# Kernel tuning notes

Measured on AMD Instinct MI355X. Metric: run time of the kernel, lower is better.

Reference implementation:

```python
import jax, jax.numpy as jnp
import numpy as np

B, C, N = 4, 256, 2048
H = 8
HD = C // H  # head_dim = 32


def setup_inputs() -> dict:
    key = jax.random.key(0)
    ks = jax.random.split(key, 5)
    s = 1.0 / np.sqrt(C)
    return {
        "x": jax.random.normal(ks[0], (B, C, 3, N), dtype=jnp.float32),
        "Wq": jax.random.normal(ks[1], (C, C), dtype=jnp.float32) * s,
        "Wk": jax.random.normal(ks[2], (C, C), dtype=jnp.float32) * s,
        "Wv": jax.random.normal(ks[3], (C, C), dtype=jnp.float32) * s,
        "Wo": jax.random.normal(ks[4], (C, C), dtype=jnp.float32) * s,
    }


def _vn_linear(W, x):
    # nn.Linear over channel axis: out[b,o,d,n] = sum_c W[o,c] x[b,c,d,n]
    return jnp.einsum('oc,bcdn->bodn', W, x)


def _heads(t):
    # [B,C,3,N] -> [B,H,N,HD,3]
    return t.reshape(B, H, HD, 3, N).transpose(0, 1, 4, 2, 3)


def reference(x, Wq, Wk, Wv, Wo):
    q = _heads(_vn_linear(Wq, x))
    k = _heads(_vn_linear(Wk, x))
    v = _heads(_vn_linear(Wv, x))
    # energy contracts over (head_dim, 3)
    energy = jnp.einsum('bhnci,bhmci->bhnm', q, k)
    attn = jax.nn.softmax(energy / np.sqrt(HD), axis=-1)
    out = jnp.einsum('bhnm,bhmci->bhnci', attn, v)
    # [B,H,N,HD,3] -> [B,C,3,N]
    out = out.transpose(0, 1, 3, 4, 2).reshape(B, C, 3, N)
    out = _vn_linear(Wo, out)
    return out + x
```

## Files before the change

kernel.cpp:

```cpp
#include <hip/hip_runtime.h>
#include <hip/hip_bf16.h>
#include <cmath>


typedef unsigned short u16;
typedef unsigned int   u32;
typedef u16   u16x8  __attribute__((ext_vector_type(8)));
typedef short s16x8  __attribute__((ext_vector_type(8)));
typedef float f32x4  __attribute__((ext_vector_type(4)));
typedef float f32x16 __attribute__((ext_vector_type(16)));

namespace {
constexpr int Nc = 2048, Fc = 96;
constexpr float SCALE_LOG2 = 0.17677669529663687f * 1.4426950408889634f;
constexpr float DEFER_THR  = 8.0f;
constexpr int KP = 104;
constexpr int VP = 40;
constexpr int VOFF = 32 * KP;
constexpr int SBUF = VOFF + 96 * VP;
}

__device__ inline float fast_exp2(float x) {
#if __has_builtin(__builtin_amdgcn_exp2f)
    return __builtin_amdgcn_exp2f(x);
#else
    return exp2f(x);
#endif
}

__device__ inline u16 f2bf(float x) {
    union { float f; unsigned u; } v; v.f = x;
    unsigned r = v.u + 0x7FFFu + ((v.u >> 16) & 1u);
    return (u16)(r >> 16);
}

__global__ __launch_bounds__(256) void wconv_kernel(
    const float* __restrict__ Wq, const float* __restrict__ Wk,
    const float* __restrict__ Wv, const float* __restrict__ Wo,
    u16* __restrict__ Wb)
{
    const int id = blockIdx.x * 256 + threadIdx.x;
    const int base = id * 8;
    const int o = base >> 8, c = base & 255;
    const int sel = o >> 8, ol = o & 255;
    const float* src = (sel == 0) ? Wq : (sel == 1) ? Wk : (sel == 2) ? Wv : Wo;
    const float sc = (sel == 0) ? SCALE_LOG2 : 1.0f;
    const float4 a = *(const float4*)&src[(size_t)ol * 256 + c];
    const float4 b = *(const float4*)&src[(size_t)ol * 256 + c + 4];
    u16x8 r;
    r[0]=f2bf(a.x*sc); r[1]=f2bf(a.y*sc); r[2]=f2bf(a.z*sc); r[3]=f2bf(a.w*sc);
    r[4]=f2bf(b.x*sc); r[5]=f2bf(b.y*sc); r[6]=f2bf(b.z*sc); r[7]=f2bf(b.w*sc);
    *(u16x8*)&Wb[(size_t)o * 256 + c] = r;
}

__global__ __launch_bounds__(256) void xt_kernel(
    const float* __restrict__ x, u16* __restrict__ xt)
{
    const int nt = blockIdx.x, ct = blockIdx.y, bi = blockIdx.z;
    const int b = bi / 3, i = bi % 3;
    const int t = (int)threadIdx.x;
    const int n0 = nt * 64, c0 = ct * 64;

    __shared__ u16 tile[64][72];

    const int n_l = t & 63;
#pragma unroll
    for (int it = 0; it < 16; ++it) {
        const int c_l = (t >> 6) + it * 4;
        tile[n_l][c_l] =
            f2bf(x[(((size_t)(b * 256 + c0 + c_l)) * 3 + i) * Nc + n0 + n_l]);
    }
    __syncthreads();
#pragma unroll
    for (int it = 0; it < 2; ++it) {
        const int idx = t + it * 256;
        const int nn = idx >> 3, part = idx & 7;
        *(u16x8*)&xt[((size_t)bi * Nc + n0 + nn) * 256 + c0 + part * 8] =
            *(const u16x8*)&tile[nn][part * 8];
    }
}

__global__ __launch_bounds__(256) void qkv_gemm_kernel(
    const u16* __restrict__ xt, const u16* __restrict__ wb,
    u16* __restrict__ Qt, u16* __restrict__ Kt, u16* __restrict__ Vf)
{
    const int nt = blockIdx.x;
    const int wy = blockIdx.y;
    const int bi = blockIdx.z;
    const int b = bi / 3, i = bi % 3;
    const int wsel = wy >> 1, ot = wy & 1;

    const u16* xs = xt + ((size_t)bi * Nc + nt * 128) * 256;
    const u16* ws = wb + (size_t)(wsel * 256 + ot * 128) * 256;

    __shared__ u16 xl[128][40];
    __shared__ u16 wl[128][40];

    const int t = (int)threadIdx.x;
    const int wv = t >> 6, lane = t & 63;
    const int g = lane >> 4, c16 = lane & 15;
    const int wr = wv >> 1, wc = wv & 1;

    f32x4 acc[4][4];
#pragma unroll
    for (int mi = 0; mi < 4; ++mi)
#pragma unroll
        for (int ni = 0; ni < 4; ++ni)
#pragma unroll
            for (int r = 0; r < 4; ++r) acc[mi][ni][r] = 0.f;

    for (int ks = 0; ks < 8; ++ks) {
        __syncthreads();
#pragma unroll
        for (int it = 0; it < 2; ++it) {
            const int idx = t + it * 256;
            const int row = idx >> 2, part = idx & 3;
            *(u16x8*)&xl[row][part * 8] =
                *(const u16x8*)&xs[(size_t)row * 256 + ks * 32 + part * 8];
            *(u16x8*)&wl[row][part * 8] =
                *(const u16x8*)&ws[(size_t)row * 256 + ks * 32 + part * 8];
        }
        __syncthreads();

        s16x8 af[4], bf[4];
        if (wsel < 2) {
#pragma unroll
            for (int mi = 0; mi < 4; ++mi) af[mi] = *(const s16x8*)&xl[wr*64 + mi*16 + c16][g*8];
#pragma unroll
            for (int ni = 0; ni < 4; ++ni) bf[ni] = *(const s16x8*)&wl[wc*64 + ni*16 + c16][g*8];
        } else {
#pragma unroll
            for (int mi = 0; mi < 4; ++mi) af[mi] = *(const s16x8*)&wl[wr*64 + mi*16 + c16][g*8];
#pragma unroll
            for (int ni = 0; ni < 4; ++ni) bf[ni] = *(const s16x8*)&xl[wc*64 + ni*16 + c16][g*8];
        }
#pragma unroll
        for (int mi = 0; mi < 4; ++mi)
#pragma unroll
            for (int ni = 0; ni < 4; ++ni)
                acc[mi][ni] = __builtin_amdgcn_mfma_f32_16x16x32_bf16(
                    af[mi], bf[ni], acc[mi][ni], 0, 0, 0);
    }

    if (wsel < 2) {
        u16* dst = wsel ? Kt : Qt;
#pragma unroll
        for (int mi = 0; mi < 4; ++mi)
#pragma unroll
            for (int ni = 0; ni < 4; ++ni) {
                const int o = ot * 128 + wc * 64 + ni * 16 + c16;
                const int h = o >> 5, cw = o & 31;
#pragma unroll
                for (int r = 0; r < 4; ++r) {
                    const int n = nt * 128 + wr * 64 + mi * 16 + g * 4 + r;
                    dst[((size_t)(b * 8 + h) * Nc + n) * Fc + i * 32 + cw] =
                        f2bf(acc[mi][ni][r]);
                }
            }
    } else {
#pragma unroll
        for (int mi = 0; mi < 4; ++mi)
#pragma unroll
            for (int ni = 0; ni < 4; ++ni) {
                const int n = nt * 128 + wc * 64 + ni * 16 + c16;
#pragma unroll
                for (int r = 0; r < 4; ++r) {
                    const int o = ot * 128 + wr * 64 + mi * 16 + g * 4 + r;
                    const int h = o >> 5, cw = o & 31;
                    Vf[((size_t)(b * 8 + h) * Fc + i * 32 + cw) * Nc + n] =
                        f2bf(acc[mi][ni][r]);
                }
            }
    }
}

__global__ __launch_bounds__(256) void attn_mfma_kernel(
    const u16* __restrict__ Qt, const u16* __restrict__ Kt,
    const u16* __restrict__ Vf, u16* __restrict__ AO)
{
    const int bid = (int)blockIdx.x;
    const int lid = (bid & 7) * 64 + (bid >> 3);
    const int bh = lid >> 4;
    const int qt = lid & 15;

    const int t    = (int)threadIdx.x;
    const int wq   = t >> 6;
    const int lane = t & 63;
    const int ql   = lane & 31;
    const int hi   = lane >> 5;

    __shared__ u16 sbuf[2][SBUF];

    const int qb = qt * 128 + wq * 32;

    s16x8 bq[6];
#pragma unroll
    for (int s6 = 0; s6 < 6; ++s6)
        bq[s6] = *(const s16x8*)&Qt[((size_t)bh * Nc + qb + ql) * Fc + s6 * 16 + hi * 8];

    const u16* g_src[3]; int g_str[3], g_dst[3];
#pragma unroll
    for (int it = 0; it < 3; ++it) {
        const int c = t + it * 256;
        if (c < 384) {
            const int row = c / 12, part = c - row * 12;
            g_src[it] = Kt + ((size_t)bh * Nc + row) * Fc + part * 8;
            g_str[it] = 32 * Fc;
            g_dst[it] = row * KP + part * 8;
        } else {
            const int c2 = c - 384, f = c2 >> 2, part = c2 & 3;
            g_src[it] = Vf + ((size_t)bh * Fc + f) * Nc + part * 8;
            g_str[it] = 32;
            g_dst[it] = VOFF + f * VP + part * 8;
        }
    }

    f32x16 acc[3];
#pragma unroll
    for (int ft = 0; ft < 3; ++ft)
#pragma unroll
        for (int r = 0; r < 16; ++r) acc[ft][r] = 0.f;
    float m_s = -INFINITY, l_s = 0.f;

    u16x8 streg[3];
#pragma unroll
    for (int it = 0; it < 3; ++it) streg[it] = *(const u16x8*)g_src[it];
#pragma unroll
    for (int it = 0; it < 3; ++it) *(u16x8*)&sbuf[0][g_dst[it]] = streg[it];
    __syncthreads();

    for (int kt = 0; kt < 64; ++kt) {
        const int cur = kt & 1;
        if (kt < 63) {
#pragma unroll
            for (int it = 0; it < 3; ++it)
                streg[it] = *(const u16x8*)(g_src[it] + (size_t)(kt + 1) * g_str[it]);
        }

        const u16* kb = &sbuf[cur][0];
        const u16* vb = &sbuf[cur][VOFF];

        f32x16 sv;
#pragma unroll
        for (int r = 0; r < 16; ++r) sv[r] = 0.f;
#pragma unroll
        for (int s6 = 0; s6 < 6; ++s6) {
            const s16x8 ka = *(const s16x8*)&kb[ql * KP + s6 * 16 + hi * 8];
            sv = __builtin_amdgcn_mfma_f32_32x32x16_bf16(ka, bq[s6], sv, 0, 0, 0);
        }

        float mloc = sv[0];
#pragma unroll
        for (int r = 1; r < 16; ++r) mloc = fmaxf(mloc, sv[r]);
        mloc = fmaxf(mloc, __shfl_xor(mloc, 32));

        if (__any(mloc > m_s + DEFER_THR)) {
            const float mnew = fmaxf(m_s, mloc);
            const float esc = fast_exp2(m_s - mnew);
            m_s = mnew; l_s *= esc;
#pragma unroll
            for (int ft = 0; ft < 3; ++ft)
#pragma unroll
                for (int r = 0; r < 16; ++r) acc[ft][r] *= esc;
        }

        float p[16]; float lsum = 0.f;
#pragma unroll
        for (int r = 0; r < 16; ++r) { p[r] = fast_exp2(sv[r] - m_s); lsum += p[r]; }
        lsum += __shfl_xor(lsum, 32);
        l_s += lsum;

        u32 pk8[8];
#pragma unroll
        for (int j = 0; j < 8; ++j)
            asm("v_cvt_pk_bf16_f32 %0, %1, %2" : "=v"(pk8[j]) : "v"(p[2*j]), "v"(p[2*j+1]));
        asm volatile("v_permlane32_swap_b32 %0, %1" : "+v"(pk8[0]), "+v"(pk8[2]));
        asm volatile("v_permlane32_swap_b32 %0, %1" : "+v"(pk8[1]), "+v"(pk8[3]));
        asm volatile("v_permlane32_swap_b32 %0, %1" : "+v"(pk8[4]), "+v"(pk8[6]));
        asm volatile("v_permlane32_swap_b32 %0, %1" : "+v"(pk8[5]), "+v"(pk8[7]));
        union U { u32 w[4]; s16x8 v; } pb0, pb1;
        pb0.w[0] = pk8[0]; pb0.w[1] = pk8[1]; pb0.w[2] = pk8[2]; pb0.w[3] = pk8[3];
        pb1.w[0] = pk8[4]; pb1.w[1] = pk8[5]; pb1.w[2] = pk8[6]; pb1.w[3] = pk8[7];

#pragma unroll
        for (int ft = 0; ft < 3; ++ft) {
            const s16x8 va0 = *(const s16x8*)&vb[(ft * 32 + ql) * VP + hi * 8];
            acc[ft] = __builtin_amdgcn_mfma_f32_32x32x16_bf16(va0, pb0.v, acc[ft], 0, 0, 0);
            const s16x8 va1 = *(const s16x8*)&vb[(ft * 32 + ql) * VP + 16 + hi * 8];
            acc[ft] = __builtin_amdgcn_mfma_f32_32x32x16_bf16(va1, pb1.v, acc[ft], 0, 0, 0);
        }

        if (kt < 63) {
#pragma unroll
            for (int it = 0; it < 3; ++it) *(u16x8*)&sbuf[cur ^ 1][g_dst[it]] = streg[it];
        }
        __syncthreads();
    }

    const float inv = 1.f / l_s;
#pragma unroll
    for (int ft = 0; ft < 3; ++ft)
#pragma unroll
        for (int r = 0; r < 16; ++r) {
            const int frow = (r & 3) + 8 * (r >> 2) + 4 * hi;
            AO[((size_t)bh * Fc + ft * 32 + frow) * Nc + qb + ql] =
                f2bf(acc[ft][r] * inv);
        }
}

__global__ __launch_bounds__(256) void aot_kernel(
    const u16* __restrict__ aof, u16* __restrict__ aot)
{
    const int nt = blockIdx.x, i = blockIdx.y, bh = blockIdx.z;
    const int b = bh >> 3, h = bh & 7;
    const int t = (int)threadIdx.x;
    const int n0 = nt * 64;

    __shared__ u16 tile[64][40];

    const int n_l = t & 63;
#pragma unroll
    for (int it = 0; it < 8; ++it) {
        const int f_l = (t >> 6) + it * 4;
        tile[n_l][f_l] = aof[((size_t)bh * Fc + i * 32 + f_l) * Nc + n0 + n_l];
    }
    __syncthreads();
    const int nn = t >> 2, part = t & 3;
    *(u16x8*)&aot[((size_t)(b * 3 + i) * Nc + n0 + nn) * 256 + h * 32 + part * 8] =
        *(const u16x8*)&tile[nn][part * 8];
}

__global__ __launch_bounds__(256) void out_gemm_kernel(
    const u16* __restrict__ aot, const u16* __restrict__ wb,
    const float* __restrict__ x, float* __restrict__ out)
{
    const int nt = blockIdx.x, ot = blockIdx.y, bi = blockIdx.z;
    const int b = bi / 3, i = bi % 3;

    const u16* bs = aot + ((size_t)bi * Nc + nt * 128) * 256;
    const u16* ws = wb + (size_t)(768 + ot * 128) * 256;

    __shared__ u16 al[128][40];
    __shared__ u16 wl[128][40];

    const int t = (int)threadIdx.x;
    const int wv = t >> 6, lane = t & 63;
    const int g = lane >> 4, c16 = lane & 15;
    const int wr = wv >> 1, wc = wv & 1;

    f32x4 acc[4][4];
#pragma unroll
    for (int mi = 0; mi < 4; ++mi)
#pragma unroll
        for (int ni = 0; ni < 4; ++ni)
#pragma unroll
            for (int r = 0; r < 4; ++r) acc[mi][ni][r] = 0.f;

    for (int ks = 0; ks < 8; ++ks) {
        __syncthreads();
#pragma unroll
        for (int it = 0; it < 2; ++it) {
            const int idx = t + it * 256;
            const int row = idx >> 2, part = idx & 3;
            *(u16x8*)&al[row][part * 8] =
                *(const u16x8*)&bs[(size_t)row * 256 + ks * 32 + part * 8];
            *(u16x8*)&wl[row][part * 8] =
                *(const u16x8*)&ws[(size_t)row * 256 + ks * 32 + part * 8];
        }
        __syncthreads();

        s16x8 af[4], bf[4];
#pragma unroll
        for (int mi = 0; mi < 4; ++mi) af[mi] = *(const s16x8*)&wl[wr*64 + mi*16 + c16][g*8];
#pragma unroll
        for (int ni = 0; ni < 4; ++ni) bf[ni] = *(const s16x8*)&al[wc*64 + ni*16 + c16][g*8];
#pragma unroll
        for (int mi = 0; mi < 4; ++mi)
#pragma unroll
            for (int ni = 0; ni < 4; ++ni)
                acc[mi][ni] = __builtin_amdgcn_mfma_f32_16x16x32_bf16(
                    af[mi], bf[ni], acc[mi][ni], 0, 0, 0);
    }

#pragma unroll
    for (int mi = 0; mi < 4; ++mi)
#pragma unroll
        for (int ni = 0; ni < 4; ++ni) {
            const int n = nt * 128 + wc * 64 + ni * 16 + c16;
#pragma unroll
            for (int r = 0; r < 4; ++r) {
                const int o = ot * 128 + wr * 64 + mi * 16 + g * 4 + r;
                const size_t idx = ((size_t)(b * 256 + o) * 3 + i) * Nc + n;
                out[idx] = x[idx] + acc[mi][ni][r];
            }
        }
}

extern "C" void kernel_launch(void* const* d_in, const int* in_sizes, int n_in,
                              void* d_out, int out_size, void* d_ws, size_t ws_size,
                              hipStream_t stream) {
    const float* x  = (const float*)d_in[0];
    const float* Wq = (const float*)d_in[1];
    const float* Wk = (const float*)d_in[2];
    const float* Wv = (const float*)d_in[3];
    const float* Wo = (const float*)d_in[4];
    float* out = (float*)d_out;

    const size_t E = (size_t)32 * Fc * Nc;
    u16* xt  = (u16*)d_ws;
    u16* wbw = xt + E;
    u16* qt  = wbw + 262144;
    u16* kt  = qt + E;
    u16* vf  = kt + E;
    u16* aof = vf + E;
    u16* aot = aof + E;

    dim3 blk(256);
    wconv_kernel    <<<dim3(128),        blk, 0, stream>>>(Wq, Wk, Wv, Wo, wbw);
    xt_kernel       <<<dim3(32, 4, 12),  blk, 0, stream>>>(x, xt);
    qkv_gemm_kernel <<<dim3(16, 6, 12),  blk, 0, stream>>>(xt, wbw, qt, kt, vf);
    attn_mfma_kernel<<<dim3(512),        blk, 0, stream>>>(qt, kt, vf, aof);
    aot_kernel      <<<dim3(32, 3, 32),  blk, 0, stream>>>(aof, aot);
    out_gemm_kernel <<<dim3(16, 2, 12),  blk, 0, stream>>>(aot, wbw, x, out);
}
```

Measured before the change: 138.2 us.

## Double KV tile size in attention, fuse output transpose, and add prefetch depth

The attention kernel now processes 64 keys per iteration with two score MFMA chains, halving the loop count and the number of barriers. Global loads are issued two tiles ahead, with stores to the alternate LDS buffer done at the top of each iteration. Tree reductions replace the serial max and sum, and s_setprio raises wave priority around the MFMA sections. The separate aot transpose kernel is removed: attention output is staged through LDS and written directly in the layout the output GEMM expects, which drops one launch and one global round trip at the cost of more LDS and registers per block.

```diff
diff --git a/kernel.cpp b/kernel.cpp
--- a/kernel.cpp
+++ b/kernel.cpp
@@ -15,8 +15,8 @@
 constexpr float SCALE_LOG2 = 0.17677669529663687f * 1.4426950408889634f;
 constexpr float DEFER_THR  = 8.0f;
 constexpr int KP = 104;
-constexpr int VP = 40;
-constexpr int VOFF = 32 * KP;
+constexpr int VP = 72;
+constexpr int VOFF = 64 * KP;
 constexpr int SBUF = VOFF + 96 * VP;
 }
 
@@ -176,7 +176,7 @@
 
 __global__ __launch_bounds__(256) void attn_mfma_kernel(
     const u16* __restrict__ Qt, const u16* __restrict__ Kt,
-    const u16* __restrict__ Vf, u16* __restrict__ AO)
+    const u16* __restrict__ Vf, u16* __restrict__ aot)
 {
     const int bid = (int)blockIdx.x;
     const int lid = (bid & 7) * 64 + (bid >> 3);
@@ -198,19 +198,20 @@
     for (int s6 = 0; s6 < 6; ++s6)
         bq[s6] = *(const s16x8*)&Qt[((size_t)bh * Nc + qb + ql) * Fc + s6 * 16 + hi * 8];
 
-    const u16* g_src[3]; int g_str[3], g_dst[3];
-#pragma unroll
-    for (int it = 0; it < 3; ++it) {
-        const int c = t + it * 256;
-        if (c < 384) {
+    const u16* g_src[6]; int g_str[6], g_dst[6];
+#pragma unroll
+    for (int it = 0; it < 6; ++it) {
+        if (it < 3) {
+            const int c = t + it * 256;
             const int row = c / 12, part = c - row * 12;
             g_src[it] = Kt + ((size_t)bh * Nc + row) * Fc + part * 8;
-            g_str[it] = 32 * Fc;
+            g_str[it] = 64 * Fc;
             g_dst[it] = row * KP + part * 8;
         } else {
-            const int c2 = c - 384, f = c2 >> 2, part = c2 & 3;
+            const int c = t + (it - 3) * 256;
+            const int f = c >> 3, part = c & 7;
             g_src[it] = Vf + ((size_t)bh * Fc + f) * Nc + part * 8;
-            g_str[it] = 32;
+            g_str[it] = 64;
             g_dst[it] = VOFF + f * VP + part * 8;
         }
     }
@@ -222,37 +223,52 @@
         for (int r = 0; r < 16; ++r) acc[ft][r] = 0.f;
     float m_s = -INFINITY, l_s = 0.f;
 
-    u16x8 streg[3];
-#pragma unroll
-    for (int it = 0; it < 3; ++it) streg[it] = *(const u16x8*)g_src[it];
-#pragma unroll
-    for (int it = 0; it < 3; ++it) *(u16x8*)&sbuf[0][g_dst[it]] = streg[it];
+    u16x8 sreg[6];
+#pragma unroll
+    for (int it = 0; it < 6; ++it) sreg[it] = *(const u16x8*)g_src[it];
+#pragma unroll
+    for (int it = 0; it < 6; ++it) *(u16x8*)&sbuf[0][g_dst[it]] = sreg[it];
+#pragma unroll
+    for (int it = 0; it < 6; ++it)
+        sreg[it] = *(const u16x8*)(g_src[it] + (size_t)g_str[it]);
     __syncthreads();
 
-    for (int kt = 0; kt < 64; ++kt) {
+    for (int kt = 0; kt < 32; ++kt) {
         const int cur = kt & 1;
-        if (kt < 63) {
-#pragma unroll
-            for (int it = 0; it < 3; ++it)
-                streg[it] = *(const u16x8*)(g_src[it] + (size_t)(kt + 1) * g_str[it]);
+        if (kt < 31) {
+#pragma unroll
+            for (int it = 0; it < 6; ++it) *(u16x8*)&sbuf[cur ^ 1][g_dst[it]] = sreg[it];
+        }
+        if (kt < 30) {
+#pragma unroll
+            for (int it = 0; it < 6; ++it)
+                sreg[it] = *(const u16x8*)(g_src[it] + (size_t)(kt + 2) * g_str[it]);
         }
 
         const u16* kb = &sbuf[cur][0];
         const u16* vb = &sbuf[cur][VOFF];
 
-        f32x16 sv;
-#pragma unroll
-        for (int r = 0; r < 16; ++r) sv[r] = 0.f;
+        f32x16 sv0, sv1;
+#pragma unroll
+        for (int r = 0; r < 16; ++r) { sv0[r] = 0.f; sv1[r] = 0.f; }
+        __builtin_amdgcn_s_setprio(1);
 #pragma unroll
         for (int s6 = 0; s6 < 6; ++s6) {
-            const s16x8 ka = *(const s16x8*)&kb[ql * KP + s6 * 16 + hi * 8];
-            sv = __builtin_amdgcn_mfma_f32_32x32x16_bf16(ka, bq[s6], sv, 0, 0, 0);
-        }
-
-        float mloc = sv[0];
-#pragma unroll
-        for (int r = 1; r < 16; ++r) mloc = fmaxf(mloc, sv[r]);
-        mloc = fmaxf(mloc, __shfl_xor(mloc, 32));
+            const s16x8 ka0 = *(const s16x8*)&kb[ql * KP + s6 * 16 + hi * 8];
+            sv0 = __builtin_amdgcn_mfma_f32_32x32x16_bf16(ka0, bq[s6], sv0, 0, 0, 0);
+            const s16x8 ka1 = *(const s16x8*)&kb[(32 + ql) * KP + s6 * 16 + hi * 8];
+            sv1 = __builtin_amdgcn_mfma_f32_32x32x16_bf16(ka1, bq[s6], sv1, 0, 0, 0);
+        }
+        __builtin_amdgcn_s_setprio(0);
+
+        float mx[16];
+#pragma unroll
+        for (int r = 0; r < 16; ++r) mx[r] = fmaxf(sv0[r], sv1[r]);
+#pragma unroll
+        for (int s = 8; s > 0; s >>= 1)
+#pragma unroll
+            for (int r = 0; r < 16; ++r) if (r < s) mx[r] = fmaxf(mx[r], mx[r + s]);
+        const float mloc = fmaxf(mx[0], __shfl_xor(mx[0], 32));
 
         if (__any(mloc > m_s + DEFER_THR)) {
             const float mnew = fmaxf(m_s, mloc);
@@ -264,70 +280,90 @@
                 for (int r = 0; r < 16; ++r) acc[ft][r] *= esc;
         }
 
-        float p[16]; float lsum = 0.f;
-#pragma unroll
-        for (int r = 0; r < 16; ++r) { p[r] = fast_exp2(sv[r] - m_s); lsum += p[r]; }
-        lsum += __shfl_xor(lsum, 32);
-        l_s += lsum;
-
-        u32 pk8[8];
-#pragma unroll
-        for (int j = 0; j < 8; ++j)
-            asm("v_cvt_pk_bf16_f32 %0, %1, %2" : "=v"(pk8[j]) : "v"(p[2*j]), "v"(p[2*j+1]));
-        asm volatile("v_permlane32_swap_b32 %0, %1" : "+v"(pk8[0]), "+v"(pk8[2]));
-        asm volatile("v_permlane32_swap_b32 %0, %1" : "+v"(pk8[1]), "+v"(pk8[3]));
-        asm volatile("v_permlane32_swap_b32 %0, %1" : "+v"(pk8[4]), "+v"(pk8[6]));
-        asm volatile("v_permlane32_swap_b32 %0, %1" : "+v"(pk8[5]), "+v"(pk8[7]));
-        union U { u32 w[4]; s16x8 v; } pb0, pb1;
-        pb0.w[0] = pk8[0]; pb0.w[1] = pk8[1]; pb0.w[2] = pk8[2]; pb0.w[3] = pk8[3];
-        pb1.w[0] = pk8[4]; pb1.w[1] = pk8[5]; pb1.w[2] = pk8[6]; pb1.w[3] = pk8[7];
-
+#pragma unroll
+        for (int r = 0; r < 16; ++r) {
+            sv0[r] = fast_exp2(sv0[r] - m_s);
+            sv1[r] = fast_exp2(sv1[r] - m_s);
+        }
+        float ls[16];
+#pragma unroll
+        for (int r = 0; r < 16; ++r) ls[r] = sv0[r] + sv1[r];
+#pragma unroll
+        for (int s = 8; s > 0; s >>= 1)
+#pragma unroll
+            for (int r = 0; r < 16; ++r) if (r < s) ls[r] += ls[r + s];
+        l_s += ls[0] + __shfl_xor(ls[0], 32);
+
+        u32 pk0[8], pk1[8];
+#pragma unroll
+        for (int j = 0; j < 8; ++j) {
+            asm("v_cvt_pk_bf16_f32 %0, %1, %2" : "=v"(pk0[j]) : "v"(sv0[2*j]), "v"(sv0[2*j+1]));
+            asm("v_cvt_pk_bf16_f32 %0, %1, %2" : "=v"(pk1[j]) : "v"(sv1[2*j]), "v"(sv1[2*j+1]));
+        }
+        asm volatile("v_permlane32_swap_b32 %0, %1" : "+v"(pk0[0]), "+v"(pk0[2]));
+        asm volatile("v_permlane32_swap_b32 %0, %1" : "+v"(pk0[1]), "+v"(pk0[3]));
+        asm volatile("v_permlane32_swap_b32 %0, %1" : "+v"(pk0[4]), "+v"(pk0[6]));
+        asm volatile("v_permlane32_swap_b32 %0, %1" : "+v"(pk0[5]), "+v"(pk0[7]));
+        asm volatile("v_permlane32_swap_b32 %0, %1" : "+v"(pk1[0]), "+v"(pk1[2]));
+        asm volatile("v_permlane32_swap_b32 %0, %1" : "+v"(pk1[1]), "+v"(pk1[3]));
+        asm volatile("v_permlane32_swap_b32 %0, %1" : "+v"(pk1[4]), "+v"(pk1[6]));
+        asm volatile("v_permlane32_swap_b32 %0, %1" : "+v"(pk1[5]), "+v"(pk1[7]));
+        union U { u32 w[4]; s16x8 v; } pb[4];
+        pb[0].w[0]=pk0[0]; pb[0].w[1]=pk0[1]; pb[0].w[2]=pk0[2]; pb[0].w[3]=pk0[3];
+        pb[1].w[0]=pk0[4]; pb[1].w[1]=pk0[5]; pb[1].w[2]=pk0[6]; pb[1].w[3]=pk0[7];
+        pb[2].w[0]=pk1[0]; pb[2].w[1]=pk1[1]; pb[2].w[2]=pk1[2]; pb[2].w[3]=pk1[3];
+        pb[3].w[0]=pk1[4]; pb[3].w[1]=pk1[5]; pb[3].w[2]=pk1[6]; pb[3].w[3]=pk1[7];
+
+        __builtin_amdgcn_s_setprio(1);
 #pragma unroll
         for (int ft = 0; ft < 3; ++ft) {
-            const s16x8 va0 = *(const s16x8*)&vb[(ft * 32 + ql) * VP + hi * 8];
-            acc[ft] = __builtin_amdgcn_mfma_f32_32x32x16_bf16(va0, pb0.v, acc[ft], 0, 0, 0);
-            const s16x8 va1 = *(const s16x8*)&vb[(ft * 32 + ql) * VP + 16 + hi * 8];
-            acc[ft] = __builtin_amdgcn_mfma_f32_32x32x16_bf16(va1, pb1.v, acc[ft], 0, 0, 0);
-        }
-
-        if (kt < 63) {
-#pragma unroll
-            for (int it = 0; it < 3; ++it) *(u16x8*)&sbuf[cur ^ 1][g_dst[it]] = streg[it];
-        }
+#pragma unroll
+            for (int ks = 0; ks < 4; ++ks) {
+                const s16x8 va = *(const s16x8*)&vb[(ft * 32 + ql) * VP + ks * 16 + hi * 8];
+                acc[ft] = __builtin_amdgcn_mfma_f32_32x32x16_bf16(va, pb[ks].v, acc[ft], 0, 0, 0);
+            }
+        }
+        __builtin_amdgcn_s_setprio(0);
+
         __syncthreads();
     }
 
     const float inv = 1.f / l_s;
+    u16* ot = &sbuf[0][0] + wq * (32 * 104);
 #pragma unroll
     for (int ft = 0; ft < 3; ++ft)
 #pragma unroll
         for (int r = 0; r < 16; ++r) {
             const int frow = (r & 3) + 8 * (r >> 2) + 4 * hi;
-            AO[((size_t)bh * Fc + ft * 32 + frow) * Nc + qb + ql] =
-                f2bf(acc[ft][r] * inv);
-        }
-}
-
-__global__ __launch_bounds__(256) void aot_kernel(
-    const u16* __restrict__ aof, u16* __restrict__ aot)
-{
-    const int nt = blockIdx.x, i = blockIdx.y, bh = blockIdx.z;
-    const int b = bh >> 3, h = bh & 7;
-    const int t = (int)threadIdx.x;
-    const int n0 = nt * 64;
-
-    __shared__ u16 tile[64][40];
-
-    const int n_l = t & 63;
-#pragma unroll
-    for (int it = 0; it < 8; ++it) {
-        const int f_l = (t >> 6) + it * 4;
-        tile[n_l][f_l] = aof[((size_t)bh * Fc + i * 32 + f_l) * Nc + n0 + n_l];
-    }
+            ot[ql * 104 + ft * 32 + frow] = f2bf(acc[ft][r] * inv);
+        }
     __syncthreads();
-    const int nn = t >> 2, part = t & 3;
-    *(u16x8*)&aot[((size_t)(b * 3 + i) * Nc + n0 + nn) * 256 + h * 32 + part * 8] =
-        *(const u16x8*)&tile[nn][part * 8];
+
+    u16x8 v6[6];
+#pragma unroll
+    for (int j = 0; j < 6; ++j)
+        v6[j] = *(const u16x8*)&ot[ql * 104 + hi * 48 + j * 8];
+
+    const int n = qb + ql;
+    const int b_ = bh >> 3, h_ = bh & 7;
+    const size_t base0 = ((size_t)(b_ * 3 + 0) * Nc + n) * 256 + h_ * 32;
+    const size_t base1 = ((size_t)(b_ * 3 + 1) * Nc + n) * 256 + h_ * 32;
+    const size_t base2 = ((size_t)(b_ * 3 + 2) * Nc + n) * 256 + h_ * 32;
+    if (hi == 0) {
+        *(u16x8*)&aot[base0 +  0] = v6[0];
+        *(u16x8*)&aot[base0 +  8] = v6[1];
+        *(u16x8*)&aot[base0 + 16] = v6[2];
+        *(u16x8*)&aot[base0 + 24] = v6[3];
+        *(u16x8*)&aot[base1 +  0] = v6[4];
+        *(u16x8*)&aot[base1 +  8] = v6[5];
+    } else {
+        *(u16x8*)&aot[base1 + 16] = v6[0];
+        *(u16x8*)&aot[base1 + 24] = v6[1];
+        *(u16x8*)&aot[base2 +  0] = v6[2];
+        *(u16x8*)&aot[base2 +  8] = v6[3];
+        *(u16x8*)&aot[base2 + 16] = v6[4];
+        *(u16x8*)&aot[base2 + 24] = v6[5];
+    }
 }
 
 __global__ __launch_bounds__(256) void out_gemm_kernel(
@@ -412,14 +448,12 @@
     u16* qt  = wbw + 262144;
     u16* kt  = qt + E;
     u16* vf  = kt + E;
-    u16* aof = vf + E;
-    u16* aot = aof + E;
+    u16* aot = vf + E;
 
     dim3 blk(256);
     wconv_kernel    <<<dim3(128),        blk, 0, stream>>>(Wq, Wk, Wv, Wo, wbw);
     xt_kernel       <<<dim3(32, 4, 12),  blk, 0, stream>>>(x, xt);
     qkv_gemm_kernel <<<dim3(16, 6, 12),  blk, 0, stream>>>(xt, wbw, qt, kt, vf);
-    attn_mfma_kernel<<<dim3(512),        blk, 0, stream>>>(qt, kt, vf, aof);
-    aot_kernel      <<<dim3(32, 3, 32),  blk, 0, stream>>>(aof, aot);
+    attn_mfma_kernel<<<dim3(512),        blk, 0, stream>>>(qt, kt, vf, aot);
     out_gemm_kernel <<<dim3(16, 2, 12),  blk, 0, stream>>>(aot, wbw, x, out);
 }
```

Result: no change. 135.6 us (-1.9%).
